# Kernel optimization log

Measured on AMD Instinct MI355X. Metric: run time of the kernel, lower is better.

The kernel has to match this reference:

```python
import jax, jax.numpy as jnp
import numpy as np
import math

B, S, D, H, MAX_LEN = 4, 1024, 1024, 16, 1024
DH = D // H  # 64

def setup_inputs() -> dict:
    key = jax.random.key(0)
    ks = jax.random.split(key, 9)
    s = 1.0 / math.sqrt(D)
    return {
        "q":  jax.random.normal(ks[0], (B, S, D), jnp.float32),
        "kv": jax.random.normal(ks[1], (B, S, D), jnp.float32),
        "Wq": jax.random.normal(ks[2], (D, D), jnp.float32) * s,
        "bq": jax.random.normal(ks[3], (D,), jnp.float32) * s,
        "Wk": jax.random.normal(ks[4], (D, D), jnp.float32) * s,
        "bk": jax.random.normal(ks[5], (D,), jnp.float32) * s,
        "Wv": jax.random.normal(ks[6], (D, D), jnp.float32) * s,
        "bv": jax.random.normal(ks[7], (D,), jnp.float32) * s,
        "Er": jax.random.normal(ks[8], (MAX_LEN, DH), jnp.float32),
    }

def _skew(QEr):
    # QEr: [B, H, S, S]. Music-Transformer skew trick:
    # pad one zero column on the left, reshape, drop first row.
    b, h, r, c = QEr.shape
    padded = jnp.pad(QEr, ((0, 0), (0, 0), (0, 0), (1, 0)))  # [b,h,r,c+1]
    reshaped = padded.reshape(b, h, c + 1, r)
    return reshaped[:, :, 1:, :]  # [b,h,r,c]

def reference(q, kv, Wq, bq, Wk, bk, Wv, bv, Er):
    b, s, d = kv.shape
    # projections (nn.Linear: x @ W + b with W stored [in,out])
    k = (kv @ Wk + bk).reshape(b, s, H, DH).transpose(0, 2, 3, 1)  # [b,h,dh,s]
    v = (kv @ Wv + bv).reshape(b, s, H, DH).transpose(0, 2, 1, 3)  # [b,h,s,dh]
    qh = (q @ Wq + bq).reshape(b, s, H, DH).transpose(0, 2, 1, 3)  # [b,h,s,dh]
    # relative position scores
    Er_t = Er[MAX_LEN - s:, :].T            # [dh, s]
    QEr = jnp.einsum('bhsd,dt->bhst', qh, Er_t)
    Srel = _skew(QEr)                        # [b,h,s,s]
    # content scores
    QK = jnp.einsum('bhsd,bhdt->bhst', qh, k)
    attn = (QK + Srel) / math.sqrt(DH)
    causal = jnp.tril(jnp.ones((s, s), dtype=bool))[None, None]
    attn = jnp.where(causal, attn, -jnp.inf)
    attn = jax.nn.softmax(attn, axis=-1)
    out = jnp.einsum('bhst,bhtd->bhsd', attn, v)
    out = out.transpose(0, 2, 1, 3).reshape(b, s, d)
    return out  # dropout is identity (p=0 / eval)
```

## Files before the change

kernel.cpp:

```cpp
#include <hip/hip_runtime.h>
#include <hip/hip_bf16.h>

typedef __bf16 bf16x8 __attribute__((ext_vector_type(8)));
typedef __bf16 bf16x4 __attribute__((ext_vector_type(4)));
typedef float  f32x4  __attribute__((ext_vector_type(4)));
typedef unsigned __attribute__((may_alias)) u32a;

#define MFMA_B16(a, b, c) __builtin_amdgcn_mfma_f32_16x16x32_bf16((a), (b), (c), 0, 0, 0)

static constexpr int Bk  = 4;
static constexpr int Sk  = 1024;
static constexpr int Dk  = 1024;
static constexpr int Hk  = 16;
static constexpr int DHk = 64;

static constexpr size_t QH_OFF = 0;
static constexpr size_t K_OFF  = 4194304;
static constexpr size_t VT_OFF = 8388608;
static constexpr size_t WT_OFF = 12582912;
static constexpr size_t ER_OFF = 15728640;
static constexpr size_t WS_ELEMS = 15794176;

__device__ __forceinline__ void load_lds16(const void* g, void* l) {
    __builtin_amdgcn_global_load_lds((const __attribute__((address_space(1))) void*)g,
                                     (__attribute__((address_space(3))) void*)l, 16, 0, 0);
}

template<int CTRL>
__device__ __forceinline__ float dppf(float x) {
    int v = __builtin_bit_cast(int, x);
    return __builtin_bit_cast(float,
        __builtin_amdgcn_update_dpp(v, v, CTRL, 0xF, 0xF, false));
}
__device__ __forceinline__ float rmax16(float x) {
    x = fmaxf(x, dppf<0x128>(x));
    x = fmaxf(x, dppf<0x124>(x));
    x = fmaxf(x, dppf<0x122>(x));
    x = fmaxf(x, dppf<0x121>(x));
    return x;
}
__device__ __forceinline__ float rsum16(float x) {
    x += dppf<0x128>(x);
    x += dppf<0x124>(x);
    x += dppf<0x122>(x);
    x += dppf<0x121>(x);
    return x;
}
__device__ __forceinline__ unsigned pk_bf16(float lo, float hi) {
    unsigned r;
    asm("v_cvt_pk_bf16_f32 %0, %1, %2" : "=v"(r) : "v"(lo), "v"(hi));
    return r;
}

__global__ void prep_kernel(const float* __restrict__ Wq, const float* __restrict__ Wk,
                            const float* __restrict__ Wv, const float* __restrict__ Er,
                            __bf16* __restrict__ wt, __bf16* __restrict__ erb)
{
    __shared__ float tile[64][65];
    const int z = blockIdx.z;
    const int tid = threadIdx.x;
    if (z == 3) {
        int idx = (blockIdx.y * 16 + blockIdx.x) * 256 + tid;
        erb[idx] = (__bf16)Er[idx];
        return;
    }
    const float* W = (z == 0) ? Wq : (z == 1 ? Wk : Wv);
    __bf16* dst = wt + (size_t)z * Dk * Dk;
    const int k0 = blockIdx.y * 64, n0 = blockIdx.x * 64;
    #pragma unroll
    for (int j = 0; j < 16; ++j) {
        int idx = tid + j * 256; int r = idx >> 6, c = idx & 63;
        tile[r][c] = W[(size_t)(k0 + r) * Dk + n0 + c];
    }
    __syncthreads();
    #pragma unroll
    for (int j = 0; j < 16; ++j) {
        int idx = tid + j * 256; int r = idx >> 6, c = idx & 63;
        dst[(size_t)(n0 + r) * Dk + k0 + c] = (__bf16)tile[c][r];
    }
}

__global__ __launch_bounds__(256) void proj_kernel(
    const float* __restrict__ Xq, const float* __restrict__ Xkv,
    const float* __restrict__ bq, const float* __restrict__ bk,
    const float* __restrict__ bv, const __bf16* __restrict__ wt,
    __bf16* __restrict__ qh, __bf16* __restrict__ kws, __bf16* __restrict__ vt)
{
    __shared__ __align__(16) float  Al[128 * 32];
    __shared__ __align__(16) __bf16 Bl[128 * 32];

    const int z = blockIdx.z;
    const float* X    = (z == 0) ? Xq : Xkv;
    const float* bias = (z == 0) ? bq : (z == 1 ? bk : bv);
    const __bf16* Wz  = wt + (size_t)z * Dk * Dk;

    const int m0   = blockIdx.x * 128;
    const int n0   = blockIdx.y * 128;
    const int tid  = threadIdx.x;
    const int lane = tid & 63;
    const int w    = tid >> 6;
    const int wr   = w >> 1, wc = w & 1;
    const int l15  = lane & 15;
    const int g    = lane >> 4;

    const float* asrc[4];
    int adst[4];
    #pragma unroll
    for (int i = 0; i < 4; ++i) {
        const int c = w * 4 + i;
        asrc[i] = X + (size_t)(m0 + c * 8 + (lane >> 3)) * Dk + (((lane & 7) ^ (lane >> 3)) << 2);
        adst[i] = c * 1024 + lane * 16;
    }
    const __bf16* bsrc[2];
    int bdst[2];
    #pragma unroll
    for (int i = 0; i < 2; ++i) {
        const int c = w * 2 + i;
        bsrc[i] = Wz + (size_t)(n0 + c * 16 + (lane >> 2)) * Dk + (((lane & 3) ^ ((lane >> 3) & 3)) << 3);
        bdst[i] = c * 1024 + lane * 16;
    }

    int aoff0[4], aoff1[4], boff[4];
    #pragma unroll
    for (int m = 0; m < 4; ++m) {
        const int row = wr * 64 + m * 16 + l15;
        aoff0[m] = row * 128 + (((2 * g)     ^ (l15 & 7)) << 4);
        aoff1[m] = row * 128 + (((2 * g + 1) ^ (l15 & 7)) << 4);
    }
    #pragma unroll
    for (int n = 0; n < 4; ++n) {
        const int row = wc * 64 + n * 16 + l15;
        boff[n] = row * 64 + ((g ^ ((l15 >> 1) & 3)) << 4);
    }

    const f32x4 fz = {0.f, 0.f, 0.f, 0.f};
    f32x4 acc[4][4];
    #pragma unroll
    for (int m = 0; m < 4; ++m)
        #pragma unroll
        for (int n = 0; n < 4; ++n) acc[m][n] = fz;

    const char* Alc = (const char*)Al;
    const char* Blc = (const char*)Bl;

    for (int ks = 0; ks < Dk / 32; ++ks) {
        #pragma unroll
        for (int i = 0; i < 4; ++i)
            load_lds16(asrc[i], (char*)Al + adst[i]);
        #pragma unroll
        for (int i = 0; i < 2; ++i)
            load_lds16(bsrc[i], (char*)Bl + bdst[i]);
        #pragma unroll
        for (int i = 0; i < 4; ++i) asrc[i] += 32;
        #pragma unroll
        for (int i = 0; i < 2; ++i) bsrc[i] += 32;
        __syncthreads();

        bf16x8 bf[4];
        #pragma unroll
        for (int n = 0; n < 4; ++n)
            bf[n] = *(const bf16x8*)(Blc + boff[n]);
        bf16x8 af[4];
        #pragma unroll
        for (int m = 0; m < 4; ++m) {
            f32x4 x0 = *(const f32x4*)(Alc + aoff0[m]);
            f32x4 x1 = *(const f32x4*)(Alc + aoff1[m]);
            bf16x8 a;
            a[0] = (__bf16)x0[0]; a[1] = (__bf16)x0[1]; a[2] = (__bf16)x0[2]; a[3] = (__bf16)x0[3];
            a[4] = (__bf16)x1[0]; a[5] = (__bf16)x1[1]; a[6] = (__bf16)x1[2]; a[7] = (__bf16)x1[3];
            af[m] = a;
        }

        #pragma unroll
        for (int m = 0; m < 4; ++m)
            #pragma unroll
            for (int n = 0; n < 4; ++n)
                acc[m][n] = MFMA_B16(af[m], bf[n], acc[m][n]);
        __syncthreads();
    }

    #pragma unroll
    for (int n = 0; n < 4; ++n) {
        const float bb = bias[n0 + wc * 64 + n * 16 + l15];
        #pragma unroll
        for (int m = 0; m < 4; ++m)
            #pragma unroll
            for (int r = 0; r < 4; ++r) acc[m][n][r] += bb;
    }

    const int b   = m0 >> 10;
    const int s0t = (m0 & 1023) + wr * 64;
    const int h   = (n0 + wc * 64) >> 6;

    if (z < 2) {
        __bf16* dst = (z == 0) ? qh : kws;
        const size_t rowbase = (size_t)(b * Hk + h) * Sk;
        #pragma unroll
        for (int m = 0; m < 4; ++m) {
            #pragma unroll
            for (int r = 0; r < 4; ++r) {
                const int s = s0t + m * 16 + g * 4 + r;
                __bf16* drow = dst + (rowbase + s) * DHk;
                #pragma unroll
                for (int n = 0; n < 4; ++n)
                    drow[n * 16 + l15] = (__bf16)acc[m][n][r];
            }
        }
    } else {
        const size_t hb = (size_t)(b * Hk + h) * DHk;
        #pragma unroll
        for (int m = 0; m < 4; ++m) {
            const int sb = s0t + m * 16 + g * 4;
            #pragma unroll
            for (int n = 0; n < 4; ++n) {
                const int dh = n * 16 + l15;
                bf16x4 pk;
                #pragma unroll
                for (int r = 0; r < 4; ++r) pk[r] = (__bf16)acc[m][n][r];
                *(bf16x4*)(vt + (hb + dh) * Sk + sb) = pk;
            }
        }
    }
}

__global__ __launch_bounds__(256, 3) void attn_kernel(
    const __bf16* __restrict__ qh, const __bf16* __restrict__ kws,
    const __bf16* __restrict__ vt, const __bf16* __restrict__ erb,
    float* __restrict__ out)
{
    __shared__ __align__(16) __bf16 Kl[2][4096];
    __shared__ __align__(16) __bf16 Vl[2][4096];
    __shared__ __align__(16) __bf16 P_lds[4][16][64];

    const int tid  = threadIdx.x;
    const int lane = tid & 63;
    const int w    = tid >> 6;
    const int l15  = lane & 15;
    const int g    = lane >> 4;

    const int lid   = blockIdx.x;
    const int bh    = lid & 63;
    const int strip = 15 - (lid >> 6);
    const int ntw   = strip + 1;
    const int sw    = strip * 64 + w * 16;

    const __bf16* kbase = kws + (size_t)bh * Sk * DHk;
    const __bf16* vbase = vt  + (size_t)bh * DHk * Sk;
    const __bf16* qbase = qh  + ((size_t)bh * Sk + sw) * DHk;

    __bf16 (*Pw)[64] = P_lds[w];

    const int trow   = tid >> 3;
    const int tslot  = tid & 7;
    const int srcoff = (tslot ^ (trow & 7)) << 3;
    char* kd0 = (char*)Kl + tid * 16;
    char* vd0 = (char*)Vl + tid * 16;

    bf16x8 aq[2];
    aq[0] = *(const bf16x8*)(qbase + l15 * DHk + g * 8);
    aq[1] = *(const bf16x8*)(qbase + l15 * DHk + 32 + g * 8);

    const f32x4 fz = {0.f, 0.f, 0.f, 0.f};
    f32x4 O[4];
    float m_[4], l_[4];
    #pragma unroll
    for (int n = 0; n < 4; ++n) O[n] = fz;
    #pragma unroll
    for (int r = 0; r < 4; ++r) { m_[r] = -1e30f; l_[r] = 0.f; }

    const float SCL = 0.125f * 1.44269504088896f;

    load_lds16(kbase + (size_t)trow * DHk + srcoff,        kd0);
    load_lds16(kbase + (size_t)(32 + trow) * DHk + srcoff, kd0 + 4096);
    load_lds16(vbase + (size_t)trow * Sk + srcoff,         vd0);
    load_lds16(vbase + (size_t)(32 + trow) * Sk + srcoff,  vd0 + 4096);

    for (int it = 0; it < ntw; ++it) {
        const int t0  = it * 64;
        const int cur = it & 1;

        __builtin_amdgcn_sched_barrier(0);
        asm volatile("s_waitcnt vmcnt(0)" ::: "memory");
        __builtin_amdgcn_sched_barrier(0);

        const int jb = t0 - sw + 1008;
        bf16x8 ec[10];
        #pragma unroll
        for (int kt = 0; kt < 2; ++kt)
            #pragma unroll
            for (int jj = 0; jj < 5; ++jj) {
                int jr = jb + jj * 16 + l15;
                jr = (jr > 1023) ? 1023 : jr;
                ec[kt * 5 + jj] = *(const bf16x8*)(erb + (size_t)jr * DHk + kt * 32 + g * 8);
            }

        __builtin_amdgcn_sched_barrier(0);
        __builtin_amdgcn_s_barrier();
        __builtin_amdgcn_sched_barrier(0);

        if (it + 1 < ntw) {
            const int t0n = t0 + 64;
            char* kd = kd0 + (cur ^ 1) * 8192;
            char* vd = vd0 + (cur ^ 1) * 8192;
            load_lds16(kbase + (size_t)(t0n + trow) * DHk + srcoff,      kd);
            load_lds16(kbase + (size_t)(t0n + 32 + trow) * DHk + srcoff, kd + 4096);
            load_lds16(vbase + (size_t)trow * Sk + t0n + srcoff,         vd);
            load_lds16(vbase + (size_t)(32 + trow) * Sk + t0n + srcoff,  vd + 4096);
        }

        const char* Kc = (const char*)Kl + cur * 8192;
        const char* Vc = (const char*)Vl + cur * 8192;

        f32x4 sc[4];
        #pragma unroll
        for (int j = 0; j < 4; ++j) sc[j] = fz;
        #pragma unroll
        for (int kt = 0; kt < 2; ++kt) {
            bf16x8 kb[4];
            #pragma unroll
            for (int j = 0; j < 4; ++j)
                kb[j] = *(const bf16x8*)(Kc + (j * 16 + l15) * 128 + ((((kt << 2) | g) ^ (l15 & 7)) << 4));
            __builtin_amdgcn_s_setprio(1);
            #pragma unroll
            for (int j = 0; j < 4; ++j)
                sc[j] = MFMA_B16(aq[kt], kb[j], sc[j]);
            __builtin_amdgcn_s_setprio(0);
        }

        f32x4 gf[5];
        #pragma unroll
        for (int jj = 0; jj < 5; ++jj) gf[jj] = fz;
        __builtin_amdgcn_s_setprio(1);
        #pragma unroll
        for (int kt = 0; kt < 2; ++kt)
            #pragma unroll
            for (int jj = 0; jj < 5; ++jj)
                gf[jj] = MFMA_B16(aq[kt], ec[kt * 5 + jj], gf[jj]);
        __builtin_amdgcn_s_setprio(0);

        #pragma unroll
        for (int r = 0; r < 4; ++r) {
            const int rr  = g * 4 + r;
            const int sft = 15 - rr;
            const int src = (g << 4) + ((l15 + sft) & 15);
            const bool hi = (l15 + sft) >= 16;
            float h[5];
            #pragma unroll
            for (int jj = 0; jj < 5; ++jj) h[jj] = __shfl(gf[jj][r], src);
            const int s = sw + rr;
            #pragma unroll
            for (int j = 0; j < 4; ++j) {
                float gval = hi ? h[j + 1] : h[j];
                float v = (sc[j][r] + gval) * SCL;
                int t = t0 + j * 16 + l15;
                sc[j][r] = (t > s) ? -1e30f : v;
            }
        }

        float mt[4];
        #pragma unroll
        for (int r = 0; r < 4; ++r)
            mt[r] = rmax16(fmaxf(fmaxf(sc[0][r], sc[1][r]), fmaxf(sc[2][r], sc[3][r])));

        bool grow = (mt[0] > m_[0] + 8.f) || (mt[1] > m_[1] + 8.f) ||
                    (mt[2] > m_[2] + 8.f) || (mt[3] > m_[3] + 8.f);
        if (__any(grow)) {
            #pragma unroll
            for (int r = 0; r < 4; ++r) {
                float mnew = fmaxf(m_[r], mt[r]);
                float scl  = exp2f(m_[r] - mnew);
                l_[r] *= scl;
                m_[r]  = mnew;
                #pragma unroll
                for (int n = 0; n < 4; ++n) O[n][r] *= scl;
            }
        }
        #pragma unroll
        for (int r = 0; r < 4; ++r) {
            float rs = 0.f;
            #pragma unroll
            for (int j = 0; j < 4; ++j) {
                float p = exp2f(sc[j][r] - m_[r]);
                sc[j][r] = p; rs += p;
            }
            l_[r] += rsum16(rs);
        }

        {
            const int p01 = l15 & 1;
            #pragma unroll
            for (int j = 0; j < 4; ++j) {
                const int slot = 2 * j + (l15 >> 3);
                #pragma unroll
                for (int h2 = 0; h2 < 2; ++h2) {
                    float a0 = sc[j][h2];
                    float a2 = sc[j][h2 + 2];
                    float b0 = dppf<0xB1>(a0);
                    float b2 = dppf<0xB1>(a2);
                    float lo = p01 ? b2 : a0;
                    float hi = p01 ? a2 : b0;
                    unsigned wd = pk_bf16(lo, hi);
                    const int row = g * 4 + h2 + (p01 ? 2 : 0);
                    const int byteoff = row * 128 + (((slot ^ (row & 7)) << 4) | ((l15 & 6) << 1));
                    *(u32a*)((char*)Pw + byteoff) = wd;
                }
            }
        }
        asm volatile("" ::: "memory");
        __builtin_amdgcn_sched_barrier(0);

        __builtin_amdgcn_s_setprio(1);
        #pragma unroll
        for (int kt = 0; kt < 2; ++kt) {
            bf16x8 pa = *(const bf16x8*)((const char*)Pw + l15 * 128 +
                                         ((((kt << 2) | g) ^ (l15 & 7)) << 4));
            #pragma unroll
            for (int n = 0; n < 4; ++n) {
                bf16x8 vbf = *(const bf16x8*)(Vc + (n * 16 + l15) * 128 + ((((kt << 2) | g) ^ (l15 & 7)) << 4));
                O[n] = MFMA_B16(pa, vbf, O[n]);
            }
        }
        __builtin_amdgcn_s_setprio(0);
    }

    const int b = bh >> 4, h = bh & 15;
    float* obase = out + ((size_t)b * Sk + sw) * Dk + h * DHk;
    #pragma unroll
    for (int r = 0; r < 4; ++r) {
        float inv = 1.f / l_[r];
        #pragma unroll
        for (int n = 0; n < 4; ++n)
            obase[(size_t)(g * 4 + r) * Dk + n * 16 + l15] = O[n][r] * inv;
    }
}

extern "C" void kernel_launch(void* const* d_in, const int* in_sizes, int n_in,
                              void* d_out, int out_size, void* d_ws, size_t ws_size,
                              hipStream_t stream)
{
    const float* q  = (const float*)d_in[0];
    const float* kv = (const float*)d_in[1];
    const float* Wq = (const float*)d_in[2];
    const float* bq = (const float*)d_in[3];
    const float* Wk = (const float*)d_in[4];
    const float* bk = (const float*)d_in[5];
    const float* Wv = (const float*)d_in[6];
    const float* bv = (const float*)d_in[7];
    const float* Er = (const float*)d_in[8];
    float* out = (float*)d_out;

    if (ws_size < WS_ELEMS * sizeof(__bf16)) return;
    __bf16* ws  = (__bf16*)d_ws;
    __bf16* qh  = ws + QH_OFF;
    __bf16* kws = ws + K_OFF;
    __bf16* vt  = ws + VT_OFF;
    __bf16* wt  = ws + WT_OFF;
    __bf16* erb = ws + ER_OFF;

    prep_kernel<<<dim3(16, 16, 4), 256, 0, stream>>>(Wq, Wk, Wv, Er, wt, erb);
    proj_kernel<<<dim3(32, 8, 3), 256, 0, stream>>>(q, kv, bq, bk, bv, wt, qh, kws, vt);
    attn_kernel<<<dim3(1024), 256, 0, stream>>>(qh, kws, vt, erb, out);
}
```

Measured before the change: 103.7 us.

## Software-pipeline QK and relative-position MFMAs one tile ahead of softmax

```diff
diff --git a/kernel.cpp b/kernel.cpp
--- a/kernel.cpp
+++ b/kernel.cpp
@@ -223,13 +223,51 @@
     }
 }
 
+__device__ __forceinline__ void front_tile(
+    const char* Kc, const __bf16* __restrict__ erb, int jb, int l15, int g,
+    const bf16x8 (&aq)[2], f32x4 (&sc)[4], f32x4 (&gf)[5])
+{
+    const f32x4 fz = {0.f, 0.f, 0.f, 0.f};
+    #pragma unroll
+    for (int j = 0; j < 4; ++j) sc[j] = fz;
+    #pragma unroll
+    for (int jj = 0; jj < 5; ++jj) gf[jj] = fz;
+    #pragma unroll
+    for (int kt = 0; kt < 2; ++kt) {
+        bf16x8 kb[4];
+        #pragma unroll
+        for (int j = 0; j < 4; ++j)
+            kb[j] = *(const bf16x8*)(Kc + (j * 16 + l15) * 128 + ((((kt << 2) | g) ^ (l15 & 7)) << 4));
+        __builtin_amdgcn_s_setprio(1);
+        #pragma unroll
+        for (int j = 0; j < 4; ++j)
+            sc[j] = MFMA_B16(aq[kt], kb[j], sc[j]);
+        __builtin_amdgcn_s_setprio(0);
+    }
+    #pragma unroll
+    for (int kt = 0; kt < 2; ++kt) {
+        bf16x8 ec[5];
+        #pragma unroll
+        for (int jj = 0; jj < 5; ++jj) {
+            int jr = jb + jj * 16 + l15;
+            jr = (jr > 1023) ? 1023 : jr;
+            ec[jj] = *(const bf16x8*)(erb + (size_t)jr * DHk + kt * 32 + g * 8);
+        }
+        __builtin_amdgcn_s_setprio(1);
+        #pragma unroll
+        for (int jj = 0; jj < 5; ++jj)
+            gf[jj] = MFMA_B16(aq[kt], ec[jj], gf[jj]);
+        __builtin_amdgcn_s_setprio(0);
+    }
+}
+
 __global__ __launch_bounds__(256, 3) void attn_kernel(
     const __bf16* __restrict__ qh, const __bf16* __restrict__ kws,
     const __bf16* __restrict__ vt, const __bf16* __restrict__ erb,
     float* __restrict__ out)
 {
     __shared__ __align__(16) __bf16 Kl[2][4096];
-    __shared__ __align__(16) __bf16 Vl[2][4096];
+    __shared__ __align__(16) __bf16 Vl[3][4096];
     __shared__ __align__(16) __bf16 P_lds[4][16][64];
 
     const int tid  = threadIdx.x;
@@ -274,69 +312,36 @@
     load_lds16(kbase + (size_t)(32 + trow) * DHk + srcoff, kd0 + 4096);
     load_lds16(vbase + (size_t)trow * Sk + srcoff,         vd0);
     load_lds16(vbase + (size_t)(32 + trow) * Sk + srcoff,  vd0 + 4096);
+    __builtin_amdgcn_sched_barrier(0);
+    asm volatile("s_waitcnt vmcnt(0)" ::: "memory");
+    __builtin_amdgcn_sched_barrier(0);
+    __builtin_amdgcn_s_barrier();
+    __builtin_amdgcn_sched_barrier(0);
+
+    f32x4 scA[4], scB[4], gf[5];
+    front_tile((const char*)Kl, erb, 1008 - sw, l15, g, aq, scA, gf);
+
+    int vcur = 0, vnxt = 1;
 
     for (int it = 0; it < ntw; ++it) {
         const int t0  = it * 64;
         const int cur = it & 1;
-
-        __builtin_amdgcn_sched_barrier(0);
-        asm volatile("s_waitcnt vmcnt(0)" ::: "memory");
-        __builtin_amdgcn_sched_barrier(0);
-
-        const int jb = t0 - sw + 1008;
-        bf16x8 ec[10];
-        #pragma unroll
-        for (int kt = 0; kt < 2; ++kt)
-            #pragma unroll
-            for (int jj = 0; jj < 5; ++jj) {
-                int jr = jb + jj * 16 + l15;
-                jr = (jr > 1023) ? 1023 : jr;
-                ec[kt * 5 + jj] = *(const bf16x8*)(erb + (size_t)jr * DHk + kt * 32 + g * 8);
-            }
-
-        __builtin_amdgcn_sched_barrier(0);
-        __builtin_amdgcn_s_barrier();
-        __builtin_amdgcn_sched_barrier(0);
-
-        if (it + 1 < ntw) {
+        const bool more = (it + 1 < ntw);
+
+        if (more) {
             const int t0n = t0 + 64;
             char* kd = kd0 + (cur ^ 1) * 8192;
-            char* vd = vd0 + (cur ^ 1) * 8192;
+            char* vd = (char*)Vl + vnxt * 8192 + tid * 16;
             load_lds16(kbase + (size_t)(t0n + trow) * DHk + srcoff,      kd);
             load_lds16(kbase + (size_t)(t0n + 32 + trow) * DHk + srcoff, kd + 4096);
             load_lds16(vbase + (size_t)trow * Sk + t0n + srcoff,         vd);
             load_lds16(vbase + (size_t)(32 + trow) * Sk + t0n + srcoff,  vd + 4096);
         }
-
-        const char* Kc = (const char*)Kl + cur * 8192;
-        const char* Vc = (const char*)Vl + cur * 8192;
-
-        f32x4 sc[4];
-        #pragma unroll
-        for (int j = 0; j < 4; ++j) sc[j] = fz;
-        #pragma unroll
-        for (int kt = 0; kt < 2; ++kt) {
-            bf16x8 kb[4];
-            #pragma unroll
-            for (int j = 0; j < 4; ++j)
-                kb[j] = *(const bf16x8*)(Kc + (j * 16 + l15) * 128 + ((((kt << 2) | g) ^ (l15 & 7)) << 4));
-            __builtin_amdgcn_s_setprio(1);
-            #pragma unroll
-            for (int j = 0; j < 4; ++j)
-                sc[j] = MFMA_B16(aq[kt], kb[j], sc[j]);
-            __builtin_amdgcn_s_setprio(0);
-        }
-
-        f32x4 gf[5];
-        #pragma unroll
-        for (int jj = 0; jj < 5; ++jj) gf[jj] = fz;
-        __builtin_amdgcn_s_setprio(1);
-        #pragma unroll
-        for (int kt = 0; kt < 2; ++kt)
-            #pragma unroll
-            for (int jj = 0; jj < 5; ++jj)
-                gf[jj] = MFMA_B16(aq[kt], ec[kt * 5 + jj], gf[jj]);
-        __builtin_amdgcn_s_setprio(0);
+        __builtin_amdgcn_sched_barrier(0);
+        asm volatile("s_waitcnt vmcnt(0)" ::: "memory");
+        __builtin_amdgcn_sched_barrier(0);
+        __builtin_amdgcn_s_barrier();
+        __builtin_amdgcn_sched_barrier(0);
 
         #pragma unroll
         for (int r = 0; r < 4; ++r) {
@@ -351,16 +356,20 @@
             #pragma unroll
             for (int j = 0; j < 4; ++j) {
                 float gval = hi ? h[j + 1] : h[j];
-                float v = (sc[j][r] + gval) * SCL;
+                float v = (scA[j][r] + gval) * SCL;
                 int t = t0 + j * 16 + l15;
-                sc[j][r] = (t > s) ? -1e30f : v;
-            }
-        }
+                scA[j][r] = (t > s) ? -1e30f : v;
+            }
+        }
+
+        if (more)
+            front_tile((const char*)Kl + (cur ^ 1) * 8192, erb,
+                       t0 + 64 - sw + 1008, l15, g, aq, scB, gf);
 
         float mt[4];
         #pragma unroll
         for (int r = 0; r < 4; ++r)
-            mt[r] = rmax16(fmaxf(fmaxf(sc[0][r], sc[1][r]), fmaxf(sc[2][r], sc[3][r])));
+            mt[r] = rmax16(fmaxf(fmaxf(scA[0][r], scA[1][r]), fmaxf(scA[2][r], scA[3][r])));
 
         bool grow = (mt[0] > m_[0] + 8.f) || (mt[1] > m_[1] + 8.f) ||
                     (mt[2] > m_[2] + 8.f) || (mt[3] > m_[3] + 8.f);
@@ -380,8 +389,8 @@
             float rs = 0.f;
             #pragma unroll
             for (int j = 0; j < 4; ++j) {
-                float p = exp2f(sc[j][r] - m_[r]);
-                sc[j][r] = p; rs += p;
+                float p = exp2f(scA[j][r] - m_[r]);
+                scA[j][r] = p; rs += p;
             }
             l_[r] += rsum16(rs);
         }
@@ -393,8 +402,8 @@
                 const int slot = 2 * j + (l15 >> 3);
                 #pragma unroll
                 for (int h2 = 0; h2 < 2; ++h2) {
-                    float a0 = sc[j][h2];
-                    float a2 = sc[j][h2 + 2];
+                    float a0 = scA[j][h2];
+                    float a2 = scA[j][h2 + 2];
                     float b0 = dppf<0xB1>(a0);
                     float b2 = dppf<0xB1>(a2);
                     float lo = p01 ? b2 : a0;
@@ -409,6 +418,7 @@
         asm volatile("" ::: "memory");
         __builtin_amdgcn_sched_barrier(0);
 
+        const char* Vc = (const char*)Vl + vcur * 8192;
         __builtin_amdgcn_s_setprio(1);
         #pragma unroll
         for (int kt = 0; kt < 2; ++kt) {
@@ -421,6 +431,13 @@
             }
         }
         __builtin_amdgcn_s_setprio(0);
+
+        if (more) {
+            #pragma unroll
+            for (int j = 0; j < 4; ++j) scA[j] = scB[j];
+        }
+        vcur = vnxt;
+        vnxt = (vnxt == 2) ? 0 : vnxt + 1;
     }
 
     const int b = bh >> 4, h = bh & 15;
```

New measurement: 108.7 us. +4.9%, slower.

## Load V fragments directly from global into registers, pad Er to drop clamping

Applied to the files above, without the earlier changes.

```diff
diff --git a/kernel.cpp b/kernel.cpp
--- a/kernel.cpp
+++ b/kernel.cpp
@@ -19,7 +19,7 @@
 static constexpr size_t VT_OFF = 8388608;
 static constexpr size_t WT_OFF = 12582912;
 static constexpr size_t ER_OFF = 15728640;
-static constexpr size_t WS_ELEMS = 15794176;
+static constexpr size_t WS_ELEMS = 15799296;
 
 __device__ __forceinline__ void load_lds16(const void* g, void* l) {
     __builtin_amdgcn_global_load_lds((const __attribute__((address_space(1))) void*)g,
@@ -62,6 +62,7 @@
     if (z == 3) {
         int idx = (blockIdx.y * 16 + blockIdx.x) * 256 + tid;
         erb[idx] = (__bf16)Er[idx];
+        if (idx < 5120) erb[65536 + idx] = (__bf16)0.f;
         return;
     }
     const float* W = (z == 0) ? Wq : (z == 1 ? Wk : Wv);
@@ -229,7 +230,6 @@
     float* __restrict__ out)
 {
     __shared__ __align__(16) __bf16 Kl[2][4096];
-    __shared__ __align__(16) __bf16 Vl[2][4096];
     __shared__ __align__(16) __bf16 P_lds[4][16][64];
 
     const int tid  = threadIdx.x;
@@ -254,7 +254,6 @@
     const int tslot  = tid & 7;
     const int srcoff = (tslot ^ (trow & 7)) << 3;
     char* kd0 = (char*)Kl + tid * 16;
-    char* vd0 = (char*)Vl + tid * 16;
 
     bf16x8 aq[2];
     aq[0] = *(const bf16x8*)(qbase + l15 * DHk + g * 8);
@@ -270,10 +269,15 @@
 
     const float SCL = 0.125f * 1.44269504088896f;
 
+    const __bf16* ecp = erb + (size_t)(1008 - sw + l15) * DHk + g * 8;
+
     load_lds16(kbase + (size_t)trow * DHk + srcoff,        kd0);
     load_lds16(kbase + (size_t)(32 + trow) * DHk + srcoff, kd0 + 4096);
-    load_lds16(vbase + (size_t)trow * Sk + srcoff,         vd0);
-    load_lds16(vbase + (size_t)(32 + trow) * Sk + srcoff,  vd0 + 4096);
+    __builtin_amdgcn_sched_barrier(0);
+    asm volatile("s_waitcnt vmcnt(0)" ::: "memory");
+    __builtin_amdgcn_sched_barrier(0);
+    __builtin_amdgcn_s_barrier();
+    __builtin_amdgcn_sched_barrier(0);
 
     for (int it = 0; it < ntw; ++it) {
         const int t0  = it * 64;
@@ -283,16 +287,18 @@
         asm volatile("s_waitcnt vmcnt(0)" ::: "memory");
         __builtin_amdgcn_sched_barrier(0);
 
-        const int jb = t0 - sw + 1008;
         bf16x8 ec[10];
         #pragma unroll
         for (int kt = 0; kt < 2; ++kt)
             #pragma unroll
-            for (int jj = 0; jj < 5; ++jj) {
-                int jr = jb + jj * 16 + l15;
-                jr = (jr > 1023) ? 1023 : jr;
-                ec[kt * 5 + jj] = *(const bf16x8*)(erb + (size_t)jr * DHk + kt * 32 + g * 8);
-            }
+            for (int jj = 0; jj < 5; ++jj)
+                ec[kt * 5 + jj] = *(const bf16x8*)(ecp + jj * 16 * DHk + kt * 32);
+        bf16x8 vb[8];
+        #pragma unroll
+        for (int kt = 0; kt < 2; ++kt)
+            #pragma unroll
+            for (int n = 0; n < 4; ++n)
+                vb[kt * 4 + n] = *(const bf16x8*)(vbase + (size_t)(n * 16 + l15) * Sk + t0 + kt * 32 + g * 8);
 
         __builtin_amdgcn_sched_barrier(0);
         __builtin_amdgcn_s_barrier();
@@ -301,15 +307,11 @@
         if (it + 1 < ntw) {
             const int t0n = t0 + 64;
             char* kd = kd0 + (cur ^ 1) * 8192;
-            char* vd = vd0 + (cur ^ 1) * 8192;
             load_lds16(kbase + (size_t)(t0n + trow) * DHk + srcoff,      kd);
             load_lds16(kbase + (size_t)(t0n + 32 + trow) * DHk + srcoff, kd + 4096);
-            load_lds16(vbase + (size_t)trow * Sk + t0n + srcoff,         vd);
-            load_lds16(vbase + (size_t)(32 + trow) * Sk + t0n + srcoff,  vd + 4096);
         }
 
         const char* Kc = (const char*)Kl + cur * 8192;
-        const char* Vc = (const char*)Vl + cur * 8192;
 
         f32x4 sc[4];
         #pragma unroll
@@ -415,12 +417,12 @@
             bf16x8 pa = *(const bf16x8*)((const char*)Pw + l15 * 128 +
                                          ((((kt << 2) | g) ^ (l15 & 7)) << 4));
             #pragma unroll
-            for (int n = 0; n < 4; ++n) {
-                bf16x8 vbf = *(const bf16x8*)(Vc + (n * 16 + l15) * 128 + ((((kt << 2) | g) ^ (l15 & 7)) << 4));
-                O[n] = MFMA_B16(pa, vbf, O[n]);
-            }
+            for (int n = 0; n < 4; ++n)
+                O[n] = MFMA_B16(pa, vb[kt * 4 + n], O[n]);
         }
         __builtin_amdgcn_s_setprio(0);
+
+        ecp += 64 * DHk;
     }
 
     const int b = bh >> 4, h = bh & 15;
```

Measured after the change: 128.9 us. +24.3%, slower.

## Widen attention key tile to 128 per iteration with larger LDS buffers

Applied to the files above, without the earlier changes.

```diff
diff --git a/kernel.cpp b/kernel.cpp
--- a/kernel.cpp
+++ b/kernel.cpp
@@ -223,14 +223,49 @@
     }
 }
 
-__global__ __launch_bounds__(256, 3) void attn_kernel(
+__device__ __forceinline__ void g_skew_half(
+    const bf16x8* ec , const bf16x8 (&aq)[2],
+    f32x4 (&scH)[4], int t0h, int sw, int l15, int g, float SCL)
+{
+    const f32x4 fz = {0.f, 0.f, 0.f, 0.f};
+    f32x4 gf[5];
+    #pragma unroll
+    for (int jj = 0; jj < 5; ++jj) gf[jj] = fz;
+    __builtin_amdgcn_s_setprio(1);
+    #pragma unroll
+    for (int jj = 0; jj < 5; ++jj) gf[jj] = MFMA_B16(aq[0], ec[jj], gf[jj]);
+    #pragma unroll
+    for (int jj = 0; jj < 5; ++jj) gf[jj] = MFMA_B16(aq[1], ec[5 + jj], gf[jj]);
+    __builtin_amdgcn_s_setprio(0);
+
+    #pragma unroll
+    for (int r = 0; r < 4; ++r) {
+        const int rr  = g * 4 + r;
+        const int sft = 15 - rr;
+        const int src = (g << 4) + ((l15 + sft) & 15);
+        const bool hi = (l15 + sft) >= 16;
+        float h[5];
+        #pragma unroll
+        for (int jj = 0; jj < 5; ++jj) h[jj] = __shfl(gf[jj][r], src);
+        const int s = sw + rr;
+        #pragma unroll
+        for (int j = 0; j < 4; ++j) {
+            float gval = hi ? h[j + 1] : h[j];
+            float v = (scH[j][r] + gval) * SCL;
+            int t = t0h + j * 16 + l15;
+            scH[j][r] = (t > s) ? -1e30f : v;
+        }
+    }
+}
+
+__global__ __launch_bounds__(256, 2) void attn_kernel(
     const __bf16* __restrict__ qh, const __bf16* __restrict__ kws,
     const __bf16* __restrict__ vt, const __bf16* __restrict__ erb,
     float* __restrict__ out)
 {
-    __shared__ __align__(16) __bf16 Kl[2][4096];
-    __shared__ __align__(16) __bf16 Vl[2][4096];
-    __shared__ __align__(16) __bf16 P_lds[4][16][64];
+    __shared__ __align__(16) __bf16 Kl[2][8192];
+    __shared__ __align__(16) __bf16 Vl[2][8192];
+    __shared__ __align__(16) __bf16 P_lds[4][16][128];
 
     const int tid  = threadIdx.x;
     const int lane = tid & 63;
@@ -241,18 +276,19 @@
     const int lid   = blockIdx.x;
     const int bh    = lid & 63;
     const int strip = 15 - (lid >> 6);
-    const int ntw   = strip + 1;
+    const int ntw   = (strip >> 1) + 1;
     const int sw    = strip * 64 + w * 16;
 
     const __bf16* kbase = kws + (size_t)bh * Sk * DHk;
     const __bf16* vbase = vt  + (size_t)bh * DHk * Sk;
     const __bf16* qbase = qh  + ((size_t)bh * Sk + sw) * DHk;
 
-    __bf16 (*Pw)[64] = P_lds[w];
-
-    const int trow   = tid >> 3;
-    const int tslot  = tid & 7;
-    const int srcoff = (tslot ^ (trow & 7)) << 3;
+    __bf16 (*Pw)[128] = P_lds[w];
+
+    const int trow = tid >> 3, tslot = tid & 7;
+    const int srcK = (tslot ^ (trow & 7)) << 3;
+    const int vrow = tid >> 4, vslot = tid & 15;
+    const int srcV = (vslot ^ vrow) << 3;
     char* kd0 = (char*)Kl + tid * 16;
     char* vd0 = (char*)Vl + tid * 16;
 
@@ -270,13 +306,20 @@
 
     const float SCL = 0.125f * 1.44269504088896f;
 
-    load_lds16(kbase + (size_t)trow * DHk + srcoff,        kd0);
-    load_lds16(kbase + (size_t)(32 + trow) * DHk + srcoff, kd0 + 4096);
-    load_lds16(vbase + (size_t)trow * Sk + srcoff,         vd0);
-    load_lds16(vbase + (size_t)(32 + trow) * Sk + srcoff,  vd0 + 4096);
+    #pragma unroll
+    for (int i = 0; i < 4; ++i)
+        load_lds16(kbase + (size_t)(i * 32 + trow) * DHk + srcK, kd0 + i * 4096);
+    #pragma unroll
+    for (int i = 0; i < 4; ++i)
+        load_lds16(vbase + (size_t)(i * 16 + vrow) * Sk + srcV, vd0 + i * 4096);
+    __builtin_amdgcn_sched_barrier(0);
+    asm volatile("s_waitcnt vmcnt(0)" ::: "memory");
+    __builtin_amdgcn_sched_barrier(0);
+    __builtin_amdgcn_s_barrier();
+    __builtin_amdgcn_sched_barrier(0);
 
     for (int it = 0; it < ntw; ++it) {
-        const int t0  = it * 64;
+        const int t0  = it * 128;
         const int cur = it & 1;
 
         __builtin_amdgcn_sched_barrier(0);
@@ -284,36 +327,41 @@
         __builtin_amdgcn_sched_barrier(0);
 
         const int jb = t0 - sw + 1008;
-        bf16x8 ec[10];
-        #pragma unroll
-        for (int kt = 0; kt < 2; ++kt)
-            #pragma unroll
-            for (int jj = 0; jj < 5; ++jj) {
-                int jr = jb + jj * 16 + l15;
-                jr = (jr > 1023) ? 1023 : jr;
-                ec[kt * 5 + jj] = *(const bf16x8*)(erb + (size_t)jr * DHk + kt * 32 + g * 8);
-            }
+        bf16x8 ec[20];
+        #pragma unroll
+        for (int hf = 0; hf < 2; ++hf)
+            #pragma unroll
+            for (int kt = 0; kt < 2; ++kt)
+                #pragma unroll
+                for (int jj = 0; jj < 5; ++jj) {
+                    int jr = jb + hf * 64 + jj * 16 + l15;
+                    jr = (jr > 1023) ? 1023 : jr;
+                    ec[hf * 10 + kt * 5 + jj] =
+                        *(const bf16x8*)(erb + (size_t)jr * DHk + kt * 32 + g * 8);
+                }
 
         __builtin_amdgcn_sched_barrier(0);
         __builtin_amdgcn_s_barrier();
         __builtin_amdgcn_sched_barrier(0);
 
         if (it + 1 < ntw) {
-            const int t0n = t0 + 64;
-            char* kd = kd0 + (cur ^ 1) * 8192;
-            char* vd = vd0 + (cur ^ 1) * 8192;
-            load_lds16(kbase + (size_t)(t0n + trow) * DHk + srcoff,      kd);
-            load_lds16(kbase + (size_t)(t0n + 32 + trow) * DHk + srcoff, kd + 4096);
-            load_lds16(vbase + (size_t)trow * Sk + t0n + srcoff,         vd);
-            load_lds16(vbase + (size_t)(32 + trow) * Sk + t0n + srcoff,  vd + 4096);
-        }
-
-        const char* Kc = (const char*)Kl + cur * 8192;
-        const char* Vc = (const char*)Vl + cur * 8192;
-
-        f32x4 sc[4];
-        #pragma unroll
-        for (int j = 0; j < 4; ++j) sc[j] = fz;
+            const int t0n = t0 + 128;
+            char* kd = kd0 + (cur ^ 1) * 16384;
+            char* vd = vd0 + (cur ^ 1) * 16384;
+            #pragma unroll
+            for (int i = 0; i < 4; ++i)
+                load_lds16(kbase + (size_t)(t0n + i * 32 + trow) * DHk + srcK, kd + i * 4096);
+            #pragma unroll
+            for (int i = 0; i < 4; ++i)
+                load_lds16(vbase + (size_t)(i * 16 + vrow) * Sk + t0n + srcV, vd + i * 4096);
+        }
+
+        const char* Kc = (const char*)Kl + cur * 16384;
+        const char* Vc = (const char*)Vl + cur * 16384;
+
+        f32x4 scA[4], scB[4];
+        #pragma unroll
+        for (int j = 0; j < 4; ++j) { scA[j] = fz; scB[j] = fz; }
         #pragma unroll
         for (int kt = 0; kt < 2; ++kt) {
             bf16x8 kb[4];
@@ -323,45 +371,28 @@
             __builtin_amdgcn_s_setprio(1);
             #pragma unroll
             for (int j = 0; j < 4; ++j)
-                sc[j] = MFMA_B16(aq[kt], kb[j], sc[j]);
+                scA[j] = MFMA_B16(aq[kt], kb[j], scA[j]);
             __builtin_amdgcn_s_setprio(0);
-        }
-
-        f32x4 gf[5];
-        #pragma unroll
-        for (int jj = 0; jj < 5; ++jj) gf[jj] = fz;
-        __builtin_amdgcn_s_setprio(1);
-        #pragma unroll
-        for (int kt = 0; kt < 2; ++kt)
-            #pragma unroll
-            for (int jj = 0; jj < 5; ++jj)
-                gf[jj] = MFMA_B16(aq[kt], ec[kt * 5 + jj], gf[jj]);
-        __builtin_amdgcn_s_setprio(0);
-
+            #pragma unroll
+            for (int j = 0; j < 4; ++j)
+                kb[j] = *(const bf16x8*)(Kc + ((j + 4) * 16 + l15) * 128 + ((((kt << 2) | g) ^ (l15 & 7)) << 4));
+            __builtin_amdgcn_s_setprio(1);
+            #pragma unroll
+            for (int j = 0; j < 4; ++j)
+                scB[j] = MFMA_B16(aq[kt], kb[j], scB[j]);
+            __builtin_amdgcn_s_setprio(0);
+        }
+
+        g_skew_half(&ec[0],  aq, scA, t0,      sw, l15, g, SCL);
+        g_skew_half(&ec[10], aq, scB, t0 + 64, sw, l15, g, SCL);
+
+        float mt[4];
         #pragma unroll
         for (int r = 0; r < 4; ++r) {
-            const int rr  = g * 4 + r;
-            const int sft = 15 - rr;
-            const int src = (g << 4) + ((l15 + sft) & 15);
-            const bool hi = (l15 + sft) >= 16;
-            float h[5];
-            #pragma unroll
-            for (int jj = 0; jj < 5; ++jj) h[jj] = __shfl(gf[jj][r], src);
-            const int s = sw + rr;
-            #pragma unroll
-            for (int j = 0; j < 4; ++j) {
-                float gval = hi ? h[j + 1] : h[j];
-                float v = (sc[j][r] + gval) * SCL;
-                int t = t0 + j * 16 + l15;
-                sc[j][r] = (t > s) ? -1e30f : v;
-            }
-        }
-
-        float mt[4];
-        #pragma unroll
-        for (int r = 0; r < 4; ++r)
-            mt[r] = rmax16(fmaxf(fmaxf(sc[0][r], sc[1][r]), fmaxf(sc[2][r], sc[3][r])));
-
+            float a = fmaxf(fmaxf(scA[0][r], scA[1][r]), fmaxf(scA[2][r], scA[3][r]));
+            float b = fmaxf(fmaxf(scB[0][r], scB[1][r]), fmaxf(scB[2][r], scB[3][r]));
+            mt[r] = rmax16(fmaxf(a, b));
+        }
         bool grow = (mt[0] > m_[0] + 8.f) || (mt[1] > m_[1] + 8.f) ||
                     (mt[2] > m_[2] + 8.f) || (mt[3] > m_[3] + 8.f);
         if (__any(grow)) {
@@ -380,8 +411,8 @@
             float rs = 0.f;
             #pragma unroll
             for (int j = 0; j < 4; ++j) {
-                float p = exp2f(sc[j][r] - m_[r]);
-                sc[j][r] = p; rs += p;
+                float p = exp2f(scA[j][r] - m_[r]); scA[j][r] = p; rs += p;
+                float q = exp2f(scB[j][r] - m_[r]); scB[j][r] = q; rs += q;
             }
             l_[r] += rsum16(rs);
         }
@@ -390,19 +421,29 @@
             const int p01 = l15 & 1;
             #pragma unroll
             for (int j = 0; j < 4; ++j) {
-                const int slot = 2 * j + (l15 >> 3);
                 #pragma unroll
                 for (int h2 = 0; h2 < 2; ++h2) {
-                    float a0 = sc[j][h2];
-                    float a2 = sc[j][h2 + 2];
-                    float b0 = dppf<0xB1>(a0);
-                    float b2 = dppf<0xB1>(a2);
-                    float lo = p01 ? b2 : a0;
-                    float hi = p01 ? a2 : b0;
-                    unsigned wd = pk_bf16(lo, hi);
                     const int row = g * 4 + h2 + (p01 ? 2 : 0);
-                    const int byteoff = row * 128 + (((slot ^ (row & 7)) << 4) | ((l15 & 6) << 1));
-                    *(u32a*)((char*)Pw + byteoff) = wd;
+                    {
+                        const int slot = 2 * j + (l15 >> 3);
+                        float a0 = scA[j][h2], a2 = scA[j][h2 + 2];
+                        float b0 = dppf<0xB1>(a0), b2 = dppf<0xB1>(a2);
+                        float lo = p01 ? b2 : a0;
+                        float hi = p01 ? a2 : b0;
+                        unsigned wd = pk_bf16(lo, hi);
+                        const int byteoff = row * 256 + (((slot ^ row) << 4) | ((l15 & 6) << 1));
+                        *(u32a*)((char*)Pw + byteoff) = wd;
+                    }
+                    {
+                        const int slot = 2 * (j + 4) + (l15 >> 3);
+                        float a0 = scB[j][h2], a2 = scB[j][h2 + 2];
+                        float b0 = dppf<0xB1>(a0), b2 = dppf<0xB1>(a2);
+                        float lo = p01 ? b2 : a0;
+                        float hi = p01 ? a2 : b0;
+                        unsigned wd = pk_bf16(lo, hi);
+                        const int byteoff = row * 256 + (((slot ^ row) << 4) | ((l15 & 6) << 1));
+                        *(u32a*)((char*)Pw + byteoff) = wd;
+                    }
                 }
             }
         }
@@ -411,12 +452,13 @@
 
         __builtin_amdgcn_s_setprio(1);
         #pragma unroll
-        for (int kt = 0; kt < 2; ++kt) {
-            bf16x8 pa = *(const bf16x8*)((const char*)Pw + l15 * 128 +
-                                         ((((kt << 2) | g) ^ (l15 & 7)) << 4));
+        for (int kt = 0; kt < 4; ++kt) {
+            bf16x8 pa = *(const bf16x8*)((const char*)Pw + l15 * 256 +
+                                         ((((kt << 2) | g) ^ l15) << 4));
             #pragma unroll
             for (int n = 0; n < 4; ++n) {
-                bf16x8 vbf = *(const bf16x8*)(Vc + (n * 16 + l15) * 128 + ((((kt << 2) | g) ^ (l15 & 7)) << 4));
+                bf16x8 vbf = *(const bf16x8*)(Vc + (n * 16 + l15) * 256 +
+                                              ((((kt << 2) | g) ^ l15) << 4));
                 O[n] = MFMA_B16(pa, vbf, O[n]);
             }
         }
```

Measured after the change: 103.5 us. No clear change (-0.2%).
